# Performance work log

Measured on AMD Instinct MI355X. Metric: run time of the kernel, lower is better.

The kernel has to match this reference:

```python
import jax, jax.numpy as jnp
import numpy as np

P = 0.8
EPS = 1e-6


def setup_inputs() -> dict:
    key = jax.random.key(0)
    k1, k2 = jax.random.split(key)
    N, C = 8192, 2048
    logits = jax.random.normal(k1, (N, C), dtype=jnp.float32)
    labels = jax.random.randint(k2, (N,), 0, C, dtype=jnp.int64)
    return {"logits": logits, "labels": labels}


def reference(logits, labels):
    N, C = logits.shape
    # targets: one-hot class indicators, [N, C]
    targets = jax.nn.one_hot(labels, C, dtype=logits.dtype)
    # class counts (first-call behavior of the stateful module): sum over batch + 1
    class_counts = targets.sum(axis=0) + 1.0  # [C]
    # seesaw mitigation factor s[i, j] = (n_j / n_i)^p if n_i > n_j else 1
    ratio = class_counts[None, :] / class_counts[:, None]  # [C, C]
    s = jnp.where(class_counts[:, None] > class_counts[None, :], ratio ** P, 1.0)
    # stable exp
    logits = logits - logits.max(axis=-1, keepdims=True)
    e = jnp.exp(logits)  # [N, C]
    # denominator[n, i] = sum_j (1 - t[n,j]) * s[i,j] * e[n,j] + e[n,i]
    # == ((1 - t) * e) @ s.T + e  -- GEMM form of the O(N*C*C) broadcast-sum
    denom = jnp.einsum('nj,ij->ni', (1.0 - targets) * e, s) + e
    sigma = e / (denom + EPS)
    loss = (-targets * jnp.log(sigma + EPS)).sum(axis=-1)  # [N]
    return loss.mean()
```

## Files before the change

### kernel.cpp

```cpp
#include <hip/hip_runtime.h>
#include <math.h>

#define NROWS 8192
#define NCLS  2048
#define NBLK  1024
#define LOG2E 1.44269504088896340736f
#define EPS   1e-6f


__global__ __launch_bounds__(256) void seesaw_rows_k(
        const float* __restrict__ logits,
        const int*   __restrict__ labels,
        float*       __restrict__ part) {
    __shared__ __align__(16) int   cnt[NCLS];
    __shared__ __align__(16) float w[NCLS];
    __shared__ float red[4];

    const int t    = threadIdx.x;
    const int lane = t & 63;
    const int wid  = t >> 6;

    const int4* lab4 = reinterpret_cast<const int4*>(labels);
    int4 L[8];
    #pragma unroll
    for (int i = 0; i < 8; ++i) L[i] = lab4[i * 256 + t];

    #pragma unroll
    for (int j = t; j < NCLS; j += 256) cnt[j] = 0;
    asm volatile("s_waitcnt lgkmcnt(0)" ::: "memory");
    __builtin_amdgcn_s_barrier();
    asm volatile("" ::: "memory");

    #pragma unroll
    for (int i = 0; i < 8; ++i) {
        atomicAdd(&cnt[L[i].x], 1);
        atomicAdd(&cnt[L[i].y], 1);
        atomicAdd(&cnt[L[i].z], 1);
        atomicAdd(&cnt[L[i].w], 1);
    }
    asm volatile("s_waitcnt lgkmcnt(0)" ::: "memory");
    __builtin_amdgcn_s_barrier();
    asm volatile("" ::: "memory");

    #pragma unroll
    for (int j = t; j < NCLS; j += 256) w[j] = 0.8f * log2f((float)(cnt[j] + 1));
    asm volatile("s_waitcnt lgkmcnt(0)" ::: "memory");
    __builtin_amdgcn_s_barrier();
    asm volatile("" ::: "memory");

    const float4* w4 = reinterpret_cast<const float4*>(w);
    float myloss = 0.0f;

    #pragma unroll
    for (int pass = 0; pass < 2; ++pass) {
        const int n = blockIdx.x * 8 + pass * 4 + wid;
        const float* rowp = logits + (size_t)n * NCLS;
        const float4* row4 = reinterpret_cast<const float4*>(rowp);

        const int y = labels[n];
        float4 v[8];
        #pragma unroll
        for (int k = 0; k < 8; ++k) v[k] = row4[k * 64 + lane];
        const float ylogit = rowp[y];

        float m = fmaxf(fmaxf(fmaxf(v[0].x, v[0].y), fmaxf(v[0].z, v[0].w)),
                        fmaxf(fmaxf(v[1].x, v[1].y), fmaxf(v[1].z, v[1].w)));
        #pragma unroll
        for (int k = 2; k < 8; ++k)
            m = fmaxf(m, fmaxf(fmaxf(v[k].x, v[k].y), fmaxf(v[k].z, v[k].w)));
        #pragma unroll
        for (int off = 32; off; off >>= 1) m = fmaxf(m, __shfl_xor(m, off, 64));

        const float wy   = w[y];
        const float base = -m * LOG2E;

        float s = 0.0f;
        #pragma unroll
        for (int k = 0; k < 8; ++k) {
            float4 wv = w4[k * 64 + lane];
            s += exp2f(fmaf(v[k].x, LOG2E, base) + fminf(wv.x - wy, 0.0f));
            s += exp2f(fmaf(v[k].y, LOG2E, base) + fminf(wv.y - wy, 0.0f));
            s += exp2f(fmaf(v[k].z, LOG2E, base) + fminf(wv.z - wy, 0.0f));
            s += exp2f(fmaf(v[k].w, LOG2E, base) + fminf(wv.w - wy, 0.0f));
        }
        #pragma unroll
        for (int off = 32; off; off >>= 1) s += __shfl_xor(s, off, 64);

        if (lane == 0) {
            float ey    = exp2f(fmaf(ylogit, LOG2E, base));
            float sigma = ey / (s + EPS);
            myloss += -logf(sigma + EPS);
        }
    }

    if (lane == 0) red[wid] = myloss;
    __syncthreads();
    if (t == 0) part[blockIdx.x] = (red[0] + red[1]) + (red[2] + red[3]);
}

__global__ __launch_bounds__(256) void finalize_k(
        const float* __restrict__ part, float* __restrict__ out) {
    const int t = threadIdx.x, lane = t & 63, wid = t >> 6;
    const float4* p4 = reinterpret_cast<const float4*>(part);
    float4 v = p4[t];
    float s = (v.x + v.y) + (v.z + v.w);
    #pragma unroll
    for (int off = 32; off; off >>= 1) s += __shfl_xor(s, off, 64);
    __shared__ float red[4];
    if (lane == 0) red[wid] = s;
    __syncthreads();
    if (t == 0) out[0] = (((red[0] + red[1]) + (red[2] + red[3]))) / (float)NROWS;
}

extern "C" void kernel_launch(void* const* d_in, const int* in_sizes, int n_in,
                              void* d_out, int out_size, void* d_ws, size_t ws_size,
                              hipStream_t stream) {
    const float* logits = (const float*)d_in[0];
    const int*   labels = (const int*)d_in[1];
    float* out  = (float*)d_out;
    float* part = (float*)d_ws;

    seesaw_rows_k<<<NBLK, 256, 0, stream>>>(logits, labels, part);
    finalize_k<<<1, 256, 0, stream>>>(part, out);
}
```

Measured before the change: 20.32 us.

## Prefetch logits rows before histogram and drop row-max stabilization

```diff
diff --git a/kernel.cpp b/kernel.cpp
--- a/kernel.cpp
+++ b/kernel.cpp
@@ -8,7 +8,7 @@
 #define EPS   1e-6f
 
 
-__global__ __launch_bounds__(256) void seesaw_rows_k(
+__global__ __launch_bounds__(256, 4) void seesaw_rows_k(
         const float* __restrict__ logits,
         const int*   __restrict__ labels,
         float*       __restrict__ part) {
@@ -24,6 +24,12 @@
     int4 L[8];
     #pragma unroll
     for (int i = 0; i < 8; ++i) L[i] = lab4[i * 256 + t];
+
+    const int n0 = blockIdx.x * 8 + wid;
+    const float4* r0 = reinterpret_cast<const float4*>(logits + (size_t)n0 * NCLS);
+    float4 va[8];
+    #pragma unroll
+    for (int k = 0; k < 8; ++k) va[k] = r0[k * 64 + lane];
 
     #pragma unroll
     for (int j = t; j < NCLS; j += 256) cnt[j] = 0;
@@ -48,52 +54,54 @@
     __builtin_amdgcn_s_barrier();
     asm volatile("" ::: "memory");
 
+    const int n1 = n0 + 4;
+    const float4* r1 = reinterpret_cast<const float4*>(logits + (size_t)n1 * NCLS);
+    float4 vb[8];
+    #pragma unroll
+    for (int k = 0; k < 8; ++k) vb[k] = r1[k * 64 + lane];
+
+    const int y0 = labels[n0];
+    const int y1 = labels[n1];
+    const float ylog0 = logits[(size_t)n0 * NCLS + y0];
+    const float ylog1 = logits[(size_t)n1 * NCLS + y1];
+
     const float4* w4 = reinterpret_cast<const float4*>(w);
-    float myloss = 0.0f;
+    const float wy0 = w[y0];
+    const float wy1 = w[y1];
+
+    float s0 = 0.0f;
+    #pragma unroll
+    for (int k = 0; k < 8; ++k) {
+        float4 wv = w4[k * 64 + lane];
+        s0 += exp2f(fmaf(va[k].x, LOG2E, fminf(wv.x - wy0, 0.0f)));
+        s0 += exp2f(fmaf(va[k].y, LOG2E, fminf(wv.y - wy0, 0.0f)));
+        s0 += exp2f(fmaf(va[k].z, LOG2E, fminf(wv.z - wy0, 0.0f)));
+        s0 += exp2f(fmaf(va[k].w, LOG2E, fminf(wv.w - wy0, 0.0f)));
+    }
+
+    float s1 = 0.0f;
+    #pragma unroll
+    for (int k = 0; k < 8; ++k) {
+        float4 wv = w4[k * 64 + lane];
+        s1 += exp2f(fmaf(vb[k].x, LOG2E, fminf(wv.x - wy1, 0.0f)));
+        s1 += exp2f(fmaf(vb[k].y, LOG2E, fminf(wv.y - wy1, 0.0f)));
+        s1 += exp2f(fmaf(vb[k].z, LOG2E, fminf(wv.z - wy1, 0.0f)));
+        s1 += exp2f(fmaf(vb[k].w, LOG2E, fminf(wv.w - wy1, 0.0f)));
+    }
 
     #pragma unroll
-    for (int pass = 0; pass < 2; ++pass) {
-        const int n = blockIdx.x * 8 + pass * 4 + wid;
-        const float* rowp = logits + (size_t)n * NCLS;
-        const float4* row4 = reinterpret_cast<const float4*>(rowp);
-
-        const int y = labels[n];
-        float4 v[8];
-        #pragma unroll
-        for (int k = 0; k < 8; ++k) v[k] = row4[k * 64 + lane];
-        const float ylogit = rowp[y];
-
-        float m = fmaxf(fmaxf(fmaxf(v[0].x, v[0].y), fmaxf(v[0].z, v[0].w)),
-                        fmaxf(fmaxf(v[1].x, v[1].y), fmaxf(v[1].z, v[1].w)));
-        #pragma unroll
-        for (int k = 2; k < 8; ++k)
-            m = fmaxf(m, fmaxf(fmaxf(v[k].x, v[k].y), fmaxf(v[k].z, v[k].w)));
-        #pragma unroll
-        for (int off = 32; off; off >>= 1) m = fmaxf(m, __shfl_xor(m, off, 64));
-
-        const float wy   = w[y];
-        const float base = -m * LOG2E;
-
-        float s = 0.0f;
-        #pragma unroll
-        for (int k = 0; k < 8; ++k) {
-            float4 wv = w4[k * 64 + lane];
-            s += exp2f(fmaf(v[k].x, LOG2E, base) + fminf(wv.x - wy, 0.0f));
-            s += exp2f(fmaf(v[k].y, LOG2E, base) + fminf(wv.y - wy, 0.0f));
-            s += exp2f(fmaf(v[k].z, LOG2E, base) + fminf(wv.z - wy, 0.0f));
-            s += exp2f(fmaf(v[k].w, LOG2E, base) + fminf(wv.w - wy, 0.0f));
-        }
-        #pragma unroll
-        for (int off = 32; off; off >>= 1) s += __shfl_xor(s, off, 64);
-
-        if (lane == 0) {
-            float ey    = exp2f(fmaf(ylogit, LOG2E, base));
-            float sigma = ey / (s + EPS);
-            myloss += -logf(sigma + EPS);
-        }
+    for (int off = 32; off; off >>= 1) {
+        s0 += __shfl_xor(s0, off, 64);
+        s1 += __shfl_xor(s1, off, 64);
     }
 
-    if (lane == 0) red[wid] = myloss;
+    if (lane == 0) {
+        float ey0 = exp2f(ylog0 * LOG2E);
+        float ey1 = exp2f(ylog1 * LOG2E);
+        float l0 = -logf(ey0 / (s0 + EPS) + EPS);
+        float l1 = -logf(ey1 / (s1 + EPS) + EPS);
+        red[wid] = l0 + l1;
+    }
     __syncthreads();
     if (t == 0) part[blockIdx.x] = (red[0] + red[1]) + (red[2] + red[3]);
 }
```

New measurement: 20.36 us. No clear change (+0.2%).
